# Kernel optimization log

Hardware: AMD Instinct MI355X
Metric: run time of the kernel (lower is better)

## Reference

```python
import jax, jax.numpy as jnp
import numpy as np

D = 256; H = 8; NL = 4; NP = 4; DH = D // H
IMG = 2048; SIDE = 256; NUM_INTERP = 2; PTS = NUM_INTERP + 1
SIDE_LENS = (32, 16, 8, 4)
LEVEL_SHAPES = ((256, 256), (128, 128), (64, 64), (32, 32))
IMG_STARTS = (0, 65536, 81920, 86016)   # level starts in full feature pyramid
VAL_STARTS = (0, 1024, 1280, 1344)      # level starts in cropped pyramid (sum=1360)


def layernorm(x, w, b, eps=1e-5):
    m = x.mean(-1, keepdims=True)
    v = ((x - m) ** 2).mean(-1, keepdims=True)
    return (x - m) * jax.lax.rsqrt(v + eps) * w + b


def pos_encode_2d(x, y, dim=128):
    # DETR-style sinusoidal 2D encoding: 64 dims for y, 64 for x, interleaved sin/cos
    half = dim // 2
    dim_t = 10000.0 ** (2.0 * (jnp.arange(half) // 2) / half)
    def enc(v):
        p = v[..., None] / dim_t
        return jnp.concatenate([jnp.sin(p[..., 0::2])[..., None],
                                jnp.cos(p[..., 1::2])[..., None]], -1).reshape(*v.shape, half)
    return jnp.concatenate([enc(y), enc(x)], -1)


def _forward(mask_flatten, tgt, query_pos, edge_coords, src_flatten, valid_ratios,
             in_proj_w, in_proj_b, out_proj_w, out_proj_b,
             norm1_w, norm1_b, norm2_w, norm2_b, norm3_w, norm3_b,
             lin0_w, lin0_b, lin1_w, lin1_b, lin2_w, lin2_b,
             off_w, off_b, attw_w, attw_b, val_w, val_b, oproj_w, oproj_b):
    E = tgt.shape[1]
    N = E * PTS
    # ---- self attention (dropout = identity, eval mode) ----
    qk = tgt + query_pos
    wq, wk, wv = jnp.split(in_proj_w, 3, 0)
    bq, bk, bv = jnp.split(in_proj_b, 3, 0)
    q = ((qk @ wq.T + bq) * (DH ** -0.5)).reshape(1, E, H, DH)
    k = (qk @ wk.T + bk).reshape(1, E, H, DH)
    v = (tgt @ wv.T + bv).reshape(1, E, H, DH)
    att = jax.nn.softmax(jnp.einsum('behd,bfhd->bhef', q, k), -1)
    sa = jnp.einsum('bhef,bfhd->behd', att, v).reshape(1, E, D) @ out_proj_w.T + out_proj_b
    x = layernorm(tgt + sa, norm2_w, norm2_b)

    # ---- geometry: interp points along edges, crop boxes, segment clipping ----
    a = edge_coords[0, :, :2]
    b = edge_coords[0, :, 2:]
    ts = jnp.arange(PTS, dtype=jnp.float32) / NUM_INTERP
    pts = (a[:, None, :] + ts[None, :, None] * (b - a)[:, None, :]).reshape(N, 2)
    ar = jnp.broadcast_to(a[:, None, :], (E, PTS, 2)).reshape(N, 2)
    br = jnp.broadcast_to(b[:, None, :], (E, PTS, 2)).reshape(N, 2)
    c = jnp.floor(pts).astype(jnp.int32)  # int() truncation, coords > 0
    cx, cy = c[:, 0], c[:, 1]
    minx = jnp.maximum(cx - SIDE // 2, 0)
    minx = jnp.where(minx + SIDE > IMG, IMG - SIDE, minx)
    miny = jnp.maximum(cy - SIDE // 2, 0)
    miny = jnp.where(miny + SIDE > IMG, IMG - SIDE, miny)
    fminx = minx.astype(jnp.float32)
    fminy = miny.astype(jnp.float32)
    d = br - ar
    def axis_clip(p0, d0, lo, hi):
        safe = jnp.where(d0 == 0, 1.0, d0)
        t1 = (lo - p0) / safe
        t2 = (hi - p0) / safe
        tlo = jnp.where(d0 == 0, 0.0, jnp.minimum(t1, t2))
        thi = jnp.where(d0 == 0, 1.0, jnp.maximum(t1, t2))
        return tlo, thi
    tlx, thx = axis_clip(ar[:, 0], d[:, 0], fminx, fminx + SIDE)
    tly, thy = axis_clip(ar[:, 1], d[:, 1], fminy, fminy + SIDE)
    t0 = jnp.maximum(jnp.maximum(tlx, tly), 0.0)
    t1 = jnp.maximum(jnp.minimum(jnp.minimum(thx, thy), 1.0), t0)
    ca = ar + t0[:, None] * d   # clipped segment first endpoint
    cb = ar + t1[:, None] * d   # clipped segment second endpoint
    pos_x = jnp.stack([ca[:, 0], cb[:, 0], cx.astype(jnp.float32)], -1)
    pos_y = jnp.stack([ca[:, 1], cb[:, 1], cy.astype(jnp.float32)], -1)
    pe = pos_encode_2d(pos_x, pos_y).reshape(N, -1)  # [N, 384]

    qfeat = jnp.broadcast_to((x + query_pos)[0][:, None, :], (E, PTS, D)).reshape(N, D)
    nq = jnp.concatenate([qfeat, pe], -1) @ lin0_w.T + lin0_b  # linear0, [N, 256]

    ref = jnp.stack([(cx.astype(jnp.float32) - fminx) / SIDE,
                     (cy.astype(jnp.float32) - fminy) / SIDE], -1)  # [N, 2]
    ref4 = ref[:, None, None, :] * valid_ratios[:, None]  # [N, 1, NL, 2]

    # ---- multi-level feature crops (gather) ----
    srcs, masks = [], []
    for l in range(NL):
        h, w = LEVEL_SHAPES[l]
        s = SIDE_LENS[l]
        ratio = IMG // w
        lx = jnp.round(fminx / ratio).astype(jnp.int32)
        ly = jnp.round(fminy / ratio).astype(jnp.int32)
        rows = ly[:, None] + jnp.arange(s)
        cols = lx[:, None] + jnp.arange(s)
        flat = (rows[:, :, None] * w + cols[:, None, :]).reshape(N, s * s)
        srcs.append(src_flatten[0, IMG_STARTS[l]:IMG_STARTS[l] + h * w][flat])
        masks.append(mask_flatten[0, IMG_STARTS[l]:IMG_STARTS[l] + h * w][flat])
    vsrc = jnp.concatenate(srcs, 1)    # [N, 1360, D]
    vmask = jnp.concatenate(masks, 1)  # [N, 1360]

    # ---- MSDeformAttn cross attention ----
    value = vsrc @ val_w.T + val_b
    value = jnp.where(vmask[..., None], 0.0, value).reshape(N, -1, H, DH)
    off = (nq @ off_w.T + off_b).reshape(N, H, NL, NP, 2)
    aw = jax.nn.softmax((nq @ attw_w.T + attw_b).reshape(N, H, NL * NP), -1).reshape(N, H, NL, NP)
    normalizer = jnp.array([[s, s] for s in SIDE_LENS], jnp.float32)  # (w, h) per crop level
    loc = ref4[:, 0, None, :, None, :] + off / normalizer[None, None, :, None, :]  # [N,H,NL,NP,2]
    n_idx = jnp.arange(N)[:, None, None]
    h_idx = jnp.arange(H)[None, :, None]
    out_acc = jnp.zeros((N, H, DH), jnp.float32)
    for l in range(NL):
        s = SIDE_LENS[l]
        vl = value[:, VAL_STARTS[l]:VAL_STARTS[l] + s * s].reshape(N, s, s, H, DH)
        g = loc[:, :, l]  # [N, H, NP, 2]
        px = g[..., 0] * s - 0.5  # grid_sample align_corners=False
        py = g[..., 1] * s - 0.5
        x0 = jnp.floor(px).astype(jnp.int32)
        y0 = jnp.floor(py).astype(jnp.int32)
        fx = px - x0
        fy = py - y0
        def tap(xi, yi):
            ok = (xi >= 0) & (xi < s) & (yi >= 0) & (yi < s)
            val = vl[n_idx, jnp.clip(yi, 0, s - 1), jnp.clip(xi, 0, s - 1), h_idx]
            return jnp.where(ok[..., None], val, 0.0)
        samp = (tap(x0, y0) * ((1 - fx) * (1 - fy))[..., None]
                + tap(x0 + 1, y0) * (fx * (1 - fy))[..., None]
                + tap(x0, y0 + 1) * ((1 - fx) * fy)[..., None]
                + tap(x0 + 1, y0 + 1) * (fx * fy)[..., None])  # [N,H,NP,DH]
        out_acc = out_acc + (aw[:, :, l, :, None] * samp).sum(2)
    ca_out = out_acc.reshape(N, D) @ oproj_w.T + oproj_b  # [N, D]

    # ---- per-edge mean pooling over interpolation samples ----
    pooled = ca_out.reshape(E, PTS, D).mean(1)[None]
    x = layernorm(x + pooled, norm1_w, norm1_b)
    # ---- FFN ----
    ffn = jax.nn.relu(x @ lin1_w.T + lin1_b) @ lin2_w.T + lin2_b
    return layernorm(x + ffn, norm3_w, norm3_b)


def setup_inputs():
    key = jax.random.key(0)
    ks = jax.random.split(key, 16)
    E = 128
    nrm = lambda k, shape, s=1.0: s * jax.random.normal(k, shape, jnp.float32)
    W = lambda k, o, i: nrm(k, (o, i), 0.02)
    theta = jax.random.uniform(ks[2], (E,), minval=0.0, maxval=2.0 * np.pi)
    start = jax.random.uniform(ks[3], (E, 2), minval=250.0, maxval=1798.0)
    end = start + 200.0 * jnp.stack([jnp.cos(theta), jnp.sin(theta)], -1)  # length 200 -> num_interp=2
    return dict(
        tgt=nrm(ks[0], (1, E, D)),
        query_pos=nrm(ks[1], (1, E, D)),
        edge_coords=jnp.concatenate([start, end], -1)[None],
        src_flatten=nrm(ks[4], (1, 87040, D)),
        mask_flatten=jnp.zeros((1, 87040), bool),
        valid_ratios=jnp.ones((1, 4, 2), jnp.float32),
        in_proj_w=W(ks[5], 3 * D, D), in_proj_b=jnp.zeros(3 * D),
        out_proj_w=W(ks[6], D, D), out_proj_b=jnp.zeros(D),
        norm1_w=jnp.ones(D), norm1_b=jnp.zeros(D),
        norm2_w=jnp.ones(D), norm2_b=jnp.zeros(D),
        norm3_w=jnp.ones(D), norm3_b=jnp.zeros(D),
        lin0_w=W(ks[7], D, 640), lin0_b=jnp.zeros(D),
        lin1_w=W(ks[8], 1024, D), lin1_b=jnp.zeros(1024),
        lin2_w=W(ks[9], D, 1024), lin2_b=jnp.zeros(D),
        off_w=W(ks[10], H * NL * NP * 2, D) * 0.1, off_b=jnp.zeros(H * NL * NP * 2),
        attw_w=W(ks[11], H * NL * NP, D), attw_b=jnp.zeros(H * NL * NP),
        val_w=W(ks[12], D, D), val_b=jnp.zeros(D),
        oproj_w=W(ks[13], D, D), oproj_b=jnp.zeros(D),
    )


def reference(tgt, query_pos, edge_coords, src_flatten, mask_flatten, valid_ratios,
              in_proj_w, in_proj_b, out_proj_w, out_proj_b,
              norm1_w, norm1_b, norm2_w, norm2_b, norm3_w, norm3_b,
              lin0_w, lin0_b, lin1_w, lin1_b, lin2_w, lin2_b,
              off_w, off_b, attw_w, attw_b, val_w, val_b, oproj_w, oproj_b):
    return _forward(mask_flatten, tgt, query_pos, edge_coords, src_flatten, valid_ratios,
                    in_proj_w, in_proj_b, out_proj_w, out_proj_b,
                    norm1_w, norm1_b, norm2_w, norm2_b, norm3_w, norm3_b,
                    lin0_w, lin0_b, lin1_w, lin1_b, lin2_w, lin2_b,
                    off_w, off_b, attw_w, attw_b, val_w, val_b, oproj_w, oproj_b)
```

## Files before the change

### kernel.cpp

```cpp
#include <hip/hip_runtime.h>
#include <math.h>


typedef unsigned int uint;

__device__ __forceinline__ float lo16(uint u) { return __uint_as_float(u << 16); }
__device__ __forceinline__ float hi16(uint u) { return __uint_as_float(u & 0xFFFF0000u); }
__device__ __forceinline__ uint bfr(float x) {
    uint u = __float_as_uint(x);
    return (u + 0x7FFFu + ((u >> 16) & 1u)) >> 16;
}

__device__ __forceinline__ float block_sum256f(float v, float* red) {
    int t = threadIdx.x;
    __syncthreads();
    #pragma unroll
    for (int off = 32; off; off >>= 1) v += __shfl_xor(v, off);
    if (t < 256 && (t & 63) == 0) red[t >> 6] = v;
    __syncthreads();
    return red[0] + red[1] + red[2] + red[3];
}

template <int K, int MI, int MO>
__device__ void gemm_unit(const float* __restrict__ IN, const float* __restrict__ IN2,
                          const float* __restrict__ W, const float* __restrict__ B,
                          float* __restrict__ OUT, int O, int OG, int u, float* smem) {
    constexpr int KC = 128;
    constexpr int LDT = KC + 4;
    float* tile = smem;
    int og = u % OG, rg = u / OG;
    int o0 = og * 8, r0 = rg * 64;
    int t = threadIdx.x;
    int r = t & 63;
    int ol = __builtin_amdgcn_readfirstlane(t >> 6);
    int oa = o0 + ol, ob = o0 + 4 + ol;
    const float* Wa = W + (size_t)oa * K;
    const float* Wb = W + (size_t)ob * K;
    float Ba = B[oa], Bb = B[ob];
    float acca = 0.f, accb = 0.f;
    for (int c = 0; c < K / KC; c++) {
        for (int idx = t; idx < 64 * KC; idx += 256) {
            int rr = idx >> 7, ii = idx & (KC - 1);
            int row = r0 + rr, col = c * KC + ii;
            float v;
            if (MI == 0) {
                v = IN[(size_t)row * K + col];
            } else {
                float tv = IN[row * 256 + col];
                v = (o0 < 512) ? tv + IN2[row * 256 + col] : tv;
            }
            tile[rr * LDT + ii] = v;
        }
        __syncthreads();
        const float4* wa4 = (const float4*)(Wa + c * KC);
        const float4* wb4 = (const float4*)(Wb + c * KC);
        const float4* trow = (const float4*)(tile + r * LDT);
        #pragma unroll
        for (int i4 = 0; i4 < KC / 4; i4++) {
            float4 x4 = trow[i4];
            float4 a4 = wa4[i4];
            float4 b4 = wb4[i4];
            acca += x4.x * a4.x; acca += x4.y * a4.y;
            acca += x4.z * a4.z; acca += x4.w * a4.w;
            accb += x4.x * b4.x; accb += x4.y * b4.y;
            accb += x4.z * b4.z; accb += x4.w * b4.w;
        }
        __syncthreads();
    }
    acca += Ba; accb += Bb;
    if (MO == 2) {
        if (oa < 256) acca *= 0.17677669529663687f;
        if (ob < 256) accb *= 0.17677669529663687f;
    }
    OUT[(size_t)(r0 + r) * O + oa] = acca;
    OUT[(size_t)(r0 + r) * O + ob] = accb;
}

__device__ void transpose_unit(const float* __restrict__ in, float* __restrict__ out,
                               int R, int C, int u, float* smem) {
    int TC = C >> 5;
    int tc = u % TC, tr = u / TC;
    int t = threadIdx.x;
    int lr = t >> 5, lc = t & 31;
    #pragma unroll
    for (int rr = 0; rr < 32; rr += 8)
        smem[(rr + lr) * 33 + lc] = in[(size_t)(tr * 32 + rr + lr) * C + tc * 32 + lc];
    __syncthreads();
    #pragma unroll
    for (int rr = 0; rr < 32; rr += 8)
        out[(size_t)(tc * 32 + rr + lr) * R + tr * 32 + lc] = smem[lc * 33 + rr + lr];
    __syncthreads();
}

__device__ void tpack_unit(const float* __restrict__ in, uint* __restrict__ P,
                           int C, int S, int F, int u, float* smem) {
    int TC = C >> 5;
    int tc = u % TC, tr = u / TC;
    int t = threadIdx.x;
    int lr = t >> 5, lc = t & 31;
    #pragma unroll
    for (int rr = 0; rr < 32; rr += 8)
        smem[(rr + lr) * 33 + lc] = in[(size_t)(tr * 32 + rr + lr) * C + tc * 32 + lc];
    __syncthreads();
    #pragma unroll
    for (int rep = 0; rep < 2; rep++) {
        int idx = rep * 256 + t;
        int c2 = idx >> 5, r = idx & 31;
        uint w0 = bfr(smem[r * 33 + 2 * c2]);
        uint w1 = bfr(smem[r * 33 + 2 * c2 + 1]);
        P[(size_t)(tc * 16 + c2) * S + F + tr * 32 + r] = (w1 << 16) | w0;
    }
    __syncthreads();
}

__global__ __launch_bounds__(256) void k_prep(const float* __restrict__ tgt,
                                              const float* __restrict__ qpos,
                                              const float* __restrict__ ipw,
                                              const float* __restrict__ ipb,
                                              const float* __restrict__ opw,
                                              const float* __restrict__ ojw,
                                              const float* __restrict__ valw,
                                              const float* __restrict__ l1w,
                                              const float* __restrict__ l2w,
                                              const float* __restrict__ l0w,
                                              const float* __restrict__ offw,
                                              const float* __restrict__ aww,
                                              float* __restrict__ qkv,
                                              float* __restrict__ opwT,
                                              float* __restrict__ ojwT,
                                              float* __restrict__ valwT,
                                              uint* __restrict__ Pl1,
                                              uint* __restrict__ Pl2,
                                              uint* __restrict__ Pl0,
                                              uint* __restrict__ Poaw) {
    __shared__ __align__(16) float smem[8448];
    int u = blockIdx.x;
    if (u < 192)       gemm_unit<256, 1, 2>(tgt, qpos, ipw, ipb, qkv, 768, 96, u, smem);
    else if (u < 256)  transpose_unit(opw, opwT, 256, 256, u - 192, smem);
    else if (u < 320)  transpose_unit(ojw, ojwT, 256, 256, u - 256, smem);
    else if (u < 384)  transpose_unit(valw, valwT, 256, 256, u - 320, smem);
    else if (u < 640)  tpack_unit(l1w, Pl1, 256, 1024, 0, u - 384, smem);
    else if (u < 896)  tpack_unit(l2w, Pl2, 1024, 256, 0, u - 640, smem);
    else if (u < 1056) tpack_unit(l0w, Pl0, 640, 256, 0, u - 896, smem);
    else if (u < 1120) tpack_unit(offw, Poaw, 256, 384, 0, u - 1056, smem);
    else               tpack_unit(aww, Poaw, 256, 384, 256, u - 1120, smem);
}

__device__ __forceinline__ void edge_geom(const float* __restrict__ ec, int e, int j,
                                          float* pxs, float* pys,
                                          float& fminx, float& fminy,
                                          float& cxf, float& cyf) {
    float ax = ec[e * 4 + 0], ay = ec[e * 4 + 1];
    float bx = ec[e * 4 + 2], by = ec[e * 4 + 3];
    float dx = bx - ax, dy = by - ay;
    float tj = 0.5f * (float)j;
    float ptx = __fadd_rn(ax, __fmul_rn(tj, dx));
    float pty = __fadd_rn(ay, __fmul_rn(tj, dy));
    cxf = floorf(ptx); cyf = floorf(pty);
    int minx = max((int)cxf - 128, 0); if (minx + 256 > 2048) minx = 2048 - 256;
    int miny = max((int)cyf - 128, 0); if (miny + 256 > 2048) miny = 2048 - 256;
    fminx = (float)minx; fminy = (float)miny;
    float tlx, thx, tly, thy;
    if (dx == 0.f) { tlx = 0.f; thx = 1.f; }
    else { float u1 = (fminx - ax) / dx, u2 = (fminx + 256.f - ax) / dx; tlx = fminf(u1, u2); thx = fmaxf(u1, u2); }
    if (dy == 0.f) { tly = 0.f; thy = 1.f; }
    else { float u1 = (fminy - ay) / dy, u2 = (fminy + 256.f - ay) / dy; tly = fminf(u1, u2); thy = fmaxf(u1, u2); }
    float t0 = fmaxf(fmaxf(tlx, tly), 0.f);
    float t1 = fmaxf(fminf(fminf(thx, thy), 1.f), t0);
    pxs[0] = __fadd_rn(ax, __fmul_rn(t0, dx)); pys[0] = __fadd_rn(ay, __fmul_rn(t0, dy));
    pxs[1] = __fadd_rn(ax, __fmul_rn(t1, dx)); pys[1] = __fadd_rn(ay, __fmul_rn(t1, dy));
    pxs[2] = cxf; pys[2] = cyf;
}

__global__ __launch_bounds__(1024) void k_edge(const float* __restrict__ qkv,
                                               const float* __restrict__ tgt,
                                               const float* __restrict__ qpos,
                                               const float* __restrict__ opwT,
                                               const float* __restrict__ opb,
                                               const float* __restrict__ n2w,
                                               const float* __restrict__ n2b,
                                               const float* __restrict__ ec,
                                               const uint* __restrict__ Pl0,
                                               const float* __restrict__ l0b,
                                               const uint* __restrict__ Poaw,
                                               const float* __restrict__ offb,
                                               const float* __restrict__ awb,
                                               float* __restrict__ x1,
                                               float* __restrict__ offatr,
                                               float* __restrict__ refxy,
                                               int* __restrict__ lxly) {
    int n = blockIdx.x, t = threadIdx.x;
    int e = n / 3, j = n - e * 3;
    __shared__ __align__(16) float SH[2880];
    float* xq   = SH;
    float* sq   = SH + 256;
    float* sS   = SH + 512;
    float* wred = SH + 1536;
    float* ssum = SH + 1552;
    float* srow = SH + 1560;
    float* part = SH + 1824;
    float* red  = SH + 2848;
    float* pe      = SH + 256;
    float* nrow    = SH + 640;
    float* partial = SH + 896;
    if (t < 256) sq[t] = qkv[e * 768 + t];
    __syncthreads();
    int h = t >> 7;
    {
        int f = t & 127;
        const float* kf = qkv + f * 768 + 256 + h * 32;
        const float* qh = sq + h * 32;
        float s = 0.f;
        #pragma unroll 8
        for (int d = 0; d < 32; d++) s += qh[d] * kf[d];
        float m = s;
        #pragma unroll
        for (int off = 32; off; off >>= 1) m = fmaxf(m, __shfl_xor(m, off));
        if ((t & 63) == 0) wred[t >> 6] = m;
        __syncthreads();
        float hm = fmaxf(wred[2 * h], wred[2 * h + 1]);
        float ev = __expf(s - hm);
        sS[t] = ev;
        float su = ev;
        #pragma unroll
        for (int off = 32; off; off >>= 1) su += __shfl_xor(su, off);
        if ((t & 63) == 0) wred[t >> 6] = su;
        __syncthreads();
        if (t < 8) ssum[t] = 1.f / (wred[2 * t] + wred[2 * t + 1]);
    }
    {
        int o = t & 255, c = t >> 8, hh = o >> 5, d = o & 31;
        float acc = 0.f;
        #pragma unroll 8
        for (int f = c * 32; f < c * 32 + 32; f++)
            acc += sS[hh * 128 + f] * qkv[f * 768 + 512 + hh * 32 + d];
        part[t] = acc;
    }
    __syncthreads();
    if (t < 256) srow[t] = (part[t] + part[256 + t] + part[512 + t] + part[768 + t]) * ssum[t >> 5];
    __syncthreads();
    {
        int o = t & 255, c = t >> 8;
        float acc = 0.f;
        #pragma unroll 8
        for (int i = c * 64; i < c * 64 + 64; i++) acc += srow[i] * opwT[(size_t)i * 256 + o];
        part[t] = acc;
    }
    __syncthreads();
    {
        float acc = 0.f;
        if (t < 256) acc = part[t] + part[256 + t] + part[512 + t] + part[768 + t] + opb[t] + tgt[e * 256 + t];
        float mean = block_sum256f(acc, red) * (1.f / 256.f);
        float d0 = acc - mean;
        float var = block_sum256f((t < 256) ? d0 * d0 : 0.f, red) * (1.f / 256.f);
        if (t < 256) {
            float xln = d0 * rsqrtf(var + 1e-5f) * n2w[t] + n2b[t];
            if (j == 0) x1[e * 256 + t] = xln;
            xq[t] = xln + qpos[e * 256 + t];
        }
    }
    if (t < 384) {
        float pxs[3], pys[3], fmx, fmy, cxf, cyf;
        edge_geom(ec, e, j, pxs, pys, fmx, fmy, cxf, cyf);
        int jj = t >> 7, tt = t & 127, i = tt & 63, kk = i >> 1;
        float invd = __expf(-(float)kk * (9.210340371976184f / 32.f));
        float vv = (tt < 64) ? pys[jj] : pxs[jj];
        float pp = vv * invd;
        pe[t] = (i & 1) ? __cosf(pp) : __sinf(pp);
    }
    if (t == 0) {
        float pxs[3], pys[3], fmx, fmy, cxf, cyf;
        edge_geom(ec, e, j, pxs, pys, fmx, fmy, cxf, cyf);
        refxy[n * 2 + 0] = (cxf - fmx) * (1.f / 256.f);
        refxy[n * 2 + 1] = (cyf - fmy) * (1.f / 256.f);
        lxly[n * 8 + 0] = (int)rintf(fmx * 0.125f);
        lxly[n * 8 + 1] = (int)rintf(fmx * 0.0625f);
        lxly[n * 8 + 2] = (int)rintf(fmx * 0.03125f);
        lxly[n * 8 + 3] = (int)rintf(fmx * 0.015625f);
        lxly[n * 8 + 4] = (int)rintf(fmy * 0.125f);
        lxly[n * 8 + 5] = (int)rintf(fmy * 0.0625f);
        lxly[n * 8 + 6] = (int)rintf(fmy * 0.03125f);
        lxly[n * 8 + 7] = (int)rintf(fmy * 0.015625f);
    }
    __syncthreads();
    {
        int o = t & 255, kc = t >> 8;
        float acc = 0.f;
        for (int tk = 0; tk < 10; tk++) {
            const float* inb = (tk < 4) ? (xq + tk * 64) : (pe + tk * 64 - 256);
            const uint* P = Pl0 + (size_t)tk * 8192 + (size_t)(kc * 8) * 256 + o;
            #pragma unroll
            for (int kk = 0; kk < 8; kk++) {
                uint u = P[kk * 256];
                acc += inb[(kc * 8 + kk) * 2] * lo16(u);
                acc += inb[(kc * 8 + kk) * 2 + 1] * hi16(u);
            }
        }
        partial[t] = acc;
    }
    __syncthreads();
    if (t < 256) nrow[t] = partial[t] + partial[256 + t] + partial[512 + t] + partial[768 + t] + l0b[t];
    __syncthreads();
    if (t < 768) {
        int o = t % 384, kc = t / 384;
        float acc = 0.f;
        for (int tk = 0; tk < 4; tk++) {
            const float* inb = nrow + tk * 64 + kc * 32;
            const uint* P = Poaw + (size_t)tk * 12288 + (size_t)(kc * 16) * 384 + o;
            #pragma unroll
            for (int kk = 0; kk < 16; kk++) {
                uint u = P[kk * 384];
                acc += inb[kk * 2] * lo16(u);
                acc += inb[kk * 2 + 1] * hi16(u);
            }
        }
        partial[t] = acc;
    }
    __syncthreads();
    if (t < 384) {
        float b = (t < 256) ? offb[t] : awb[t - 256];
        offatr[(size_t)n * 384 + t] = partial[t] + partial[384 + t] + b;
    }
}

__global__ __launch_bounds__(1024) void k_sample(const float* __restrict__ offatr,
                                                 const float* __restrict__ refxy,
                                                 const float* __restrict__ vr,
                                                 const int* __restrict__ lxly,
                                                 const float* __restrict__ src,
                                                 const unsigned char* __restrict__ mask,
                                                 const float* __restrict__ valwT,
                                                 const float* __restrict__ valb,
                                                 float* __restrict__ ca) {
    int n = blockIdx.x, t = threadIdx.x;
    __shared__ float sl[128];
    __shared__ float sm[8], sinv[8];
    __shared__ float sw[512];
    __shared__ int   sg[512];
    __shared__ int   rk[512];
    __shared__ int   ulist[512];
    __shared__ int   wtot[16];
    __shared__ float uw[512 * 8];
    __shared__ float agg[8 * 256];
    __shared__ float pcs[64];
    __shared__ float pagg[1024];

    if (t < 128) sl[t] = offatr[(size_t)n * 384 + 256 + t];
    #pragma unroll
    for (int z = 0; z < 4; z++) uw[z * 1024 + t] = 0.f;
    __syncthreads();
    if (t < 8) {
        float m = -1e30f;
        for (int i = 0; i < 16; i++) m = fmaxf(m, sl[t * 16 + i]);
        float s = 0.f;
        for (int i = 0; i < 16; i++) s += __expf(sl[t * 16 + i] - m);
        sm[t] = m; sinv[t] = 1.f / s;
    }
    __syncthreads();
    if (t < 512) {
        int l = t >> 7, rem = t & 127;
        int h = rem >> 4, pp = (rem >> 2) & 3, tap = t & 3;
        int s = 32 >> l, wl = 256 >> l;
        const int img_starts[4] = {0, 65536, 81920, 86016};
        float a = __expf(sl[h * 16 + l * 4 + pp] - sm[h]) * sinv[h];
        float slv = (float)s;
        float gx = refxy[n * 2 + 0] * vr[l * 2 + 0] + offatr[(size_t)n * 384 + h * 32 + l * 8 + pp * 2 + 0] / slv;
        float gy = refxy[n * 2 + 1] * vr[l * 2 + 1] + offatr[(size_t)n * 384 + h * 32 + l * 8 + pp * 2 + 1] / slv;
        float px = gx * slv - 0.5f, py = gy * slv - 0.5f;
        float x0 = floorf(px), y0 = floorf(py);
        float fx = px - x0, fy = py - y0;
        int xi = (int)x0 + (tap & 1), yi = (int)y0 + (tap >> 1);
        float wtt = ((tap & 1) ? fx : (1.f - fx)) * ((tap >> 1) ? fy : (1.f - fy));
        int g = -1;
        if (xi >= 0 && xi < s && yi >= 0 && yi < s) {
            int col = lxly[n * 8 + l] + xi;
            int row = lxly[n * 8 + 4 + l] + yi;
            g = img_starts[l] + row * wl + col;
            if (mask[g]) g = -1;
        }
        sw[t] = a * wtt;
        sg[t] = g;
    }
    __syncthreads();
    int fi = -1;
    if (t < 512) {
        int g = sg[t];
        if (g >= 0) {
            fi = t;
            int base = t & ~127;
            for (int jj = base; jj < t; jj++) if (sg[jj] == g) { fi = jj; break; }
        }
    }
    bool islead = (fi == t);
    unsigned long long bal = __ballot(islead);
    int lane = t & 63, wid = t >> 6;
    if ((t & 63) == 0) wtot[wid] = __popcll(bal);
    __syncthreads();
    int woff = 0, U = 0;
    #pragma unroll
    for (int w = 0; w < 8; w++) {
        int c = wtot[w];
        if (w < wid) woff += c;
        U += c;
    }
    if (islead) {
        int r = woff + __popcll(bal & ((1ULL << lane) - 1ULL));
        rk[t] = r;
        ulist[r] = sg[t];
    }
    __syncthreads();
    if (fi >= 0) {
        int h = (t >> 4) & 7;
        atomicAdd(&uw[rk[fi] * 8 + h], sw[t]);
    }
    __syncthreads();
    {
        int ch = t & 255, q = t >> 8;
        float a0 = 0.f, a1 = 0.f;
        for (int u = 0; u < U; u++) {
            int g = ulist[u];
            float v = src[(size_t)g * 256 + ch];
            a0 += uw[u * 8 + 2 * q] * v;
            a1 += uw[u * 8 + 2 * q + 1] * v;
        }
        agg[(2 * q) * 256 + ch] = a0;
        agg[(2 * q + 1) * 256 + ch] = a1;
    }
    if (t < 64) {
        int h = t >> 3, p = t & 7;
        float s = 0.f;
        for (int u = p; u < U; u += 8) s += uw[u * 8 + h];
        pcs[t] = s;
    }
    __syncthreads();
    {
        int h = t >> 7, rem = t & 127, o = rem & 31, kc = rem >> 5;
        const float* ag = agg + h * 256 + kc * 64;
        const float* w = valwT + (size_t)(kc * 64) * 256 + h * 32 + o;
        float pv = 0.f;
        #pragma unroll 8
        for (int i = 0; i < 64; i++) pv += ag[i] * w[(size_t)i * 256];
        pagg[t] = pv;
    }
    __syncthreads();
    if (t < 256) {
        int h = t >> 5, o = t & 31;
        float cs = pcs[h * 8 + 0] + pcs[h * 8 + 1] + pcs[h * 8 + 2] + pcs[h * 8 + 3]
                 + pcs[h * 8 + 4] + pcs[h * 8 + 5] + pcs[h * 8 + 6] + pcs[h * 8 + 7];
        float r = pagg[h * 128 + o] + pagg[h * 128 + 32 + o] + pagg[h * 128 + 64 + o] + pagg[h * 128 + 96 + o];
        ca[(size_t)n * 256 + h * 32 + o] = r + cs * valb[h * 32 + o];
    }
}

__global__ __launch_bounds__(1024) void k_tail(const float* __restrict__ ca,
                                               const float* __restrict__ x1,
                                               const float* __restrict__ ojwT,
                                               const float* __restrict__ ojb,
                                               const float* __restrict__ n1w,
                                               const float* __restrict__ n1b,
                                               const uint* __restrict__ Pl1,
                                               const float* __restrict__ l1b,
                                               const uint* __restrict__ Pl2,
                                               const float* __restrict__ l2b,
                                               const float* __restrict__ n3w,
                                               const float* __restrict__ n3b,
                                               float* __restrict__ out) {
    int e = blockIdx.x, t = threadIdx.x;
    __shared__ float row[256], red[8], x2s[256], h1s[1024], part[1024];
    if (t < 256)
        row[t] = (ca[(3 * e) * 256 + t] + ca[(3 * e + 1) * 256 + t] + ca[(3 * e + 2) * 256 + t]) * (1.f / 3.f);
    __syncthreads();
    {
        int o = t & 255, c = t >> 8;
        float acc = 0.f;
        #pragma unroll 8
        for (int i = c * 64; i < c * 64 + 64; i++) acc += row[i] * ojwT[(size_t)i * 256 + o];
        part[t] = acc;
    }
    __syncthreads();
    {
        float acc = 0.f;
        if (t < 256) acc = part[t] + part[256 + t] + part[512 + t] + part[768 + t] + ojb[t] + x1[e * 256 + t];
        float mean = block_sum256f(acc, red) * (1.f / 256.f);
        float d0 = acc - mean;
        float var = block_sum256f((t < 256) ? d0 * d0 : 0.f, red) * (1.f / 256.f);
        if (t < 256) x2s[t] = d0 * rsqrtf(var + 1e-5f) * n1w[t] + n1b[t];
    }
    __syncthreads();
    {
        float acc = l1b[t];
        #pragma unroll 8
        for (int k2 = 0; k2 < 128; k2++) {
            uint u = Pl1[(size_t)k2 * 1024 + t];
            acc += x2s[2 * k2] * lo16(u);
            acc += x2s[2 * k2 + 1] * hi16(u);
        }
        h1s[t] = fmaxf(acc, 0.f);
    }
    __syncthreads();
    {
        int o = t & 255, c = t >> 8;
        float acc = 0.f;
        #pragma unroll 8
        for (int k2 = c * 128; k2 < c * 128 + 128; k2++) {
            uint u = Pl2[(size_t)k2 * 256 + o];
            acc += h1s[2 * k2] * lo16(u);
            acc += h1s[2 * k2 + 1] * hi16(u);
        }
        part[t] = acc;
    }
    __syncthreads();
    {
        float acc = 0.f;
        if (t < 256) acc = part[t] + part[256 + t] + part[512 + t] + part[768 + t] + l2b[t] + x2s[t];
        float mean = block_sum256f(acc, red) * (1.f / 256.f);
        float d0 = acc - mean;
        float var = block_sum256f((t < 256) ? d0 * d0 : 0.f, red) * (1.f / 256.f);
        if (t < 256) out[e * 256 + t] = d0 * rsqrtf(var + 1e-5f) * n3w[t] + n3b[t];
    }
}

extern "C" void kernel_launch(void* const* d_in, const int* in_sizes, int n_in,
                              void* d_out, int out_size, void* d_ws, size_t ws_size,
                              hipStream_t stream) {
    (void)in_sizes; (void)n_in; (void)out_size; (void)ws_size;
    const float* tgt  = (const float*)d_in[0];
    const float* qpos = (const float*)d_in[1];
    const float* ec   = (const float*)d_in[2];
    const float* src  = (const float*)d_in[3];
    const unsigned char* mask = (const unsigned char*)d_in[4];
    const float* vr   = (const float*)d_in[5];
    const float* ipw  = (const float*)d_in[6];
    const float* ipb  = (const float*)d_in[7];
    const float* opw  = (const float*)d_in[8];
    const float* opb  = (const float*)d_in[9];
    const float* n1w  = (const float*)d_in[10];
    const float* n1b  = (const float*)d_in[11];
    const float* n2w  = (const float*)d_in[12];
    const float* n2b  = (const float*)d_in[13];
    const float* n3w  = (const float*)d_in[14];
    const float* n3b  = (const float*)d_in[15];
    const float* l0w  = (const float*)d_in[16];
    const float* l0b  = (const float*)d_in[17];
    const float* l1w  = (const float*)d_in[18];
    const float* l1b  = (const float*)d_in[19];
    const float* l2w  = (const float*)d_in[20];
    const float* l2b  = (const float*)d_in[21];
    const float* offw = (const float*)d_in[22];
    const float* offb = (const float*)d_in[23];
    const float* aww  = (const float*)d_in[24];
    const float* awb  = (const float*)d_in[25];
    const float* valw = (const float*)d_in[26];
    const float* valb = (const float*)d_in[27];
    const float* ojw  = (const float*)d_in[28];
    const float* ojb  = (const float*)d_in[29];

    float* ws     = (float*)d_ws;
    float* qkv    = ws;
    float* x1     = ws + 98304;
    float* offatr = ws + 131072;
    float* ca     = ws + 278528;
    float* refxy  = ws + 376832;
    int*   lxly   = (int*)(ws + 377600);
    float* opwT   = ws + 380672;
    float* ojwT   = ws + 446208;
    float* valwT  = ws + 511744;
    uint*  Pl1    = (uint*)(ws + 577280);
    uint*  Pl2    = (uint*)(ws + 708352);
    uint*  Pl0    = (uint*)(ws + 839424);
    uint*  Poaw   = (uint*)(ws + 921344);

    k_prep<<<1152, 256, 0, stream>>>(tgt, qpos, ipw, ipb, opw, ojw, valw, l1w, l2w,
                                     l0w, offw, aww,
                                     qkv, opwT, ojwT, valwT, Pl1, Pl2, Pl0, Poaw);
    k_edge<<<384, 1024, 0, stream>>>(qkv, tgt, qpos, opwT, opb, n2w, n2b, ec,
                                     Pl0, l0b, Poaw, offb, awb,
                                     x1, offatr, refxy, lxly);
    k_sample<<<384, 1024, 0, stream>>>(offatr, refxy, vr, lxly, src, mask, valwT, valb, ca);
    k_tail<<<128, 1024, 0, stream>>>(ca, x1, ojwT, ojb, n1w, n1b, Pl1, l1b, Pl2, l2b, n3w, n3b, (float*)d_out);
}
```

Measured before the change: 264.5 us.

## Fuse sampling into edge kernel and defer value projection to tail after pooling

Merges the deformable-sampling kernel into the edge kernel so offsets, attention weights, reference points and level origins stay in shared memory instead of going through global memory. The value projection is moved into the tail kernel: per-point aggregated raw features (8x256) are written out, averaged over the three points of each edge, and projected once per edge rather than once per point. This saves one launch and cuts the value-projection work by a factor of three. In exchange the intermediate buffer grows eightfold and the fused kernel needs more shared memory.

```diff
diff --git a/kernel.cpp b/kernel.cpp
--- a/kernel.cpp
+++ b/kernel.cpp
@@ -185,13 +185,15 @@
                                                const uint* __restrict__ Poaw,
                                                const float* __restrict__ offb,
                                                const float* __restrict__ awb,
+                                               const float* __restrict__ vr,
+                                               const float* __restrict__ src,
+                                               const unsigned char* __restrict__ mask,
                                                float* __restrict__ x1,
-                                               float* __restrict__ offatr,
-                                               float* __restrict__ refxy,
-                                               int* __restrict__ lxly) {
+                                               float* __restrict__ aggb,
+                                               float* __restrict__ csumb) {
     int n = blockIdx.x, t = threadIdx.x;
     int e = n / 3, j = n - e * 3;
-    __shared__ __align__(16) float SH[2880];
+    __shared__ __align__(16) float SH[5056];
     float* xq   = SH;
     float* sq   = SH + 256;
     float* sS   = SH + 512;
@@ -203,6 +205,12 @@
     float* pe      = SH + 256;
     float* nrow    = SH + 640;
     float* partial = SH + 896;
+    float* offa = SH;
+    float* sw   = SH + 384;
+    float* uw   = SH + 896;
+    float* pcs  = SH + 4992;
+    __shared__ int   sg[512], rk[512], ulist[512], wtot[16], slx[8];
+    __shared__ float sm[8], sinv[8], sref[2];
     if (t < 256) sq[t] = qkv[e * 768 + t];
     __syncthreads();
     int h = t >> 7;
@@ -271,16 +279,16 @@
     if (t == 0) {
         float pxs[3], pys[3], fmx, fmy, cxf, cyf;
         edge_geom(ec, e, j, pxs, pys, fmx, fmy, cxf, cyf);
-        refxy[n * 2 + 0] = (cxf - fmx) * (1.f / 256.f);
-        refxy[n * 2 + 1] = (cyf - fmy) * (1.f / 256.f);
-        lxly[n * 8 + 0] = (int)rintf(fmx * 0.125f);
-        lxly[n * 8 + 1] = (int)rintf(fmx * 0.0625f);
-        lxly[n * 8 + 2] = (int)rintf(fmx * 0.03125f);
-        lxly[n * 8 + 3] = (int)rintf(fmx * 0.015625f);
-        lxly[n * 8 + 4] = (int)rintf(fmy * 0.125f);
-        lxly[n * 8 + 5] = (int)rintf(fmy * 0.0625f);
-        lxly[n * 8 + 6] = (int)rintf(fmy * 0.03125f);
-        lxly[n * 8 + 7] = (int)rintf(fmy * 0.015625f);
+        sref[0] = (cxf - fmx) * (1.f / 256.f);
+        sref[1] = (cyf - fmy) * (1.f / 256.f);
+        slx[0] = (int)rintf(fmx * 0.125f);
+        slx[1] = (int)rintf(fmx * 0.0625f);
+        slx[2] = (int)rintf(fmx * 0.03125f);
+        slx[3] = (int)rintf(fmx * 0.015625f);
+        slx[4] = (int)rintf(fmy * 0.125f);
+        slx[5] = (int)rintf(fmy * 0.0625f);
+        slx[6] = (int)rintf(fmy * 0.03125f);
+        slx[7] = (int)rintf(fmy * 0.015625f);
     }
     __syncthreads();
     {
@@ -317,55 +325,33 @@
         partial[t] = acc;
     }
     __syncthreads();
+    float offav = 0.f;
     if (t < 384) {
         float b = (t < 256) ? offb[t] : awb[t - 256];
-        offatr[(size_t)n * 384 + t] = partial[t] + partial[384 + t] + b;
-    }
-}
-
-__global__ __launch_bounds__(1024) void k_sample(const float* __restrict__ offatr,
-                                                 const float* __restrict__ refxy,
-                                                 const float* __restrict__ vr,
-                                                 const int* __restrict__ lxly,
-                                                 const float* __restrict__ src,
-                                                 const unsigned char* __restrict__ mask,
-                                                 const float* __restrict__ valwT,
-                                                 const float* __restrict__ valb,
-                                                 float* __restrict__ ca) {
-    int n = blockIdx.x, t = threadIdx.x;
-    __shared__ float sl[128];
-    __shared__ float sm[8], sinv[8];
-    __shared__ float sw[512];
-    __shared__ int   sg[512];
-    __shared__ int   rk[512];
-    __shared__ int   ulist[512];
-    __shared__ int   wtot[16];
-    __shared__ float uw[512 * 8];
-    __shared__ float agg[8 * 256];
-    __shared__ float pcs[64];
-    __shared__ float pagg[1024];
-
-    if (t < 128) sl[t] = offatr[(size_t)n * 384 + 256 + t];
+        offav = partial[t] + partial[384 + t] + b;
+    }
+    __syncthreads();
+    if (t < 384) offa[t] = offav;
     #pragma unroll
     for (int z = 0; z < 4; z++) uw[z * 1024 + t] = 0.f;
     __syncthreads();
     if (t < 8) {
         float m = -1e30f;
-        for (int i = 0; i < 16; i++) m = fmaxf(m, sl[t * 16 + i]);
+        for (int i = 0; i < 16; i++) m = fmaxf(m, offa[256 + t * 16 + i]);
         float s = 0.f;
-        for (int i = 0; i < 16; i++) s += __expf(sl[t * 16 + i] - m);
+        for (int i = 0; i < 16; i++) s += __expf(offa[256 + t * 16 + i] - m);
         sm[t] = m; sinv[t] = 1.f / s;
     }
     __syncthreads();
     if (t < 512) {
         int l = t >> 7, rem = t & 127;
-        int h = rem >> 4, pp = (rem >> 2) & 3, tap = t & 3;
+        int hh = rem >> 4, pp = (rem >> 2) & 3, tap = t & 3;
         int s = 32 >> l, wl = 256 >> l;
         const int img_starts[4] = {0, 65536, 81920, 86016};
-        float a = __expf(sl[h * 16 + l * 4 + pp] - sm[h]) * sinv[h];
+        float a = __expf(offa[256 + hh * 16 + l * 4 + pp] - sm[hh]) * sinv[hh];
         float slv = (float)s;
-        float gx = refxy[n * 2 + 0] * vr[l * 2 + 0] + offatr[(size_t)n * 384 + h * 32 + l * 8 + pp * 2 + 0] / slv;
-        float gy = refxy[n * 2 + 1] * vr[l * 2 + 1] + offatr[(size_t)n * 384 + h * 32 + l * 8 + pp * 2 + 1] / slv;
+        float gx = sref[0] * vr[l * 2 + 0] + offa[hh * 32 + l * 8 + pp * 2 + 0] / slv;
+        float gy = sref[1] * vr[l * 2 + 1] + offa[hh * 32 + l * 8 + pp * 2 + 1] / slv;
         float px = gx * slv - 0.5f, py = gy * slv - 0.5f;
         float x0 = floorf(px), y0 = floorf(py);
         float fx = px - x0, fy = py - y0;
@@ -373,8 +359,8 @@
         float wtt = ((tap & 1) ? fx : (1.f - fx)) * ((tap >> 1) ? fy : (1.f - fy));
         int g = -1;
         if (xi >= 0 && xi < s && yi >= 0 && yi < s) {
-            int col = lxly[n * 8 + l] + xi;
-            int row = lxly[n * 8 + 4 + l] + yi;
+            int col = slx[l] + xi;
+            int row = slx[4 + l] + yi;
             g = img_starts[l] + row * wl + col;
             if (mask[g]) g = -1;
         }
@@ -410,8 +396,8 @@
     }
     __syncthreads();
     if (fi >= 0) {
-        int h = (t >> 4) & 7;
-        atomicAdd(&uw[rk[fi] * 8 + h], sw[t]);
+        int hh = (t >> 4) & 7;
+        atomicAdd(&uw[rk[fi] * 8 + hh], sw[t]);
     }
     __syncthreads();
     {
@@ -423,37 +409,28 @@
             a0 += uw[u * 8 + 2 * q] * v;
             a1 += uw[u * 8 + 2 * q + 1] * v;
         }
-        agg[(2 * q) * 256 + ch] = a0;
-        agg[(2 * q + 1) * 256 + ch] = a1;
+        aggb[(size_t)n * 2048 + (2 * q) * 256 + ch] = a0;
+        aggb[(size_t)n * 2048 + (2 * q + 1) * 256 + ch] = a1;
     }
     if (t < 64) {
-        int h = t >> 3, p = t & 7;
+        int hh = t >> 3, p = t & 7;
         float s = 0.f;
-        for (int u = p; u < U; u += 8) s += uw[u * 8 + h];
+        for (int u = p; u < U; u += 8) s += uw[u * 8 + hh];
         pcs[t] = s;
     }
     __syncthreads();
-    {
-        int h = t >> 7, rem = t & 127, o = rem & 31, kc = rem >> 5;
-        const float* ag = agg + h * 256 + kc * 64;
-        const float* w = valwT + (size_t)(kc * 64) * 256 + h * 32 + o;
-        float pv = 0.f;
-        #pragma unroll 8
-        for (int i = 0; i < 64; i++) pv += ag[i] * w[(size_t)i * 256];
-        pagg[t] = pv;
-    }
-    __syncthreads();
-    if (t < 256) {
-        int h = t >> 5, o = t & 31;
-        float cs = pcs[h * 8 + 0] + pcs[h * 8 + 1] + pcs[h * 8 + 2] + pcs[h * 8 + 3]
-                 + pcs[h * 8 + 4] + pcs[h * 8 + 5] + pcs[h * 8 + 6] + pcs[h * 8 + 7];
-        float r = pagg[h * 128 + o] + pagg[h * 128 + 32 + o] + pagg[h * 128 + 64 + o] + pagg[h * 128 + 96 + o];
-        ca[(size_t)n * 256 + h * 32 + o] = r + cs * valb[h * 32 + o];
-    }
-}
-
-__global__ __launch_bounds__(1024) void k_tail(const float* __restrict__ ca,
+    if (t < 8) {
+        float cs = pcs[t * 8 + 0] + pcs[t * 8 + 1] + pcs[t * 8 + 2] + pcs[t * 8 + 3]
+                 + pcs[t * 8 + 4] + pcs[t * 8 + 5] + pcs[t * 8 + 6] + pcs[t * 8 + 7];
+        csumb[n * 8 + t] = cs;
+    }
+}
+
+__global__ __launch_bounds__(1024) void k_tail(const float* __restrict__ aggb,
+                                               const float* __restrict__ csumb,
                                                const float* __restrict__ x1,
+                                               const float* __restrict__ valwT,
+                                               const float* __restrict__ valb,
                                                const float* __restrict__ ojwT,
                                                const float* __restrict__ ojb,
                                                const float* __restrict__ n1w,
@@ -466,9 +443,28 @@
                                                const float* __restrict__ n3b,
                                                float* __restrict__ out) {
     int e = blockIdx.x, t = threadIdx.x;
-    __shared__ float row[256], red[8], x2s[256], h1s[1024], part[1024];
+    __shared__ float pooledA[2048], csm[8], red[8], row[256], x2s[256], h1s[1024], part[1024];
+    #pragma unroll
+    for (int k = 0; k < 2; k++) {
+        int i = k * 1024 + t;
+        pooledA[i] = (aggb[(size_t)(3 * e) * 2048 + i] + aggb[(size_t)(3 * e + 1) * 2048 + i]
+                    + aggb[(size_t)(3 * e + 2) * 2048 + i]) * (1.f / 3.f);
+    }
+    if (t < 8)
+        csm[t] = (csumb[(3 * e) * 8 + t] + csumb[(3 * e + 1) * 8 + t] + csumb[(3 * e + 2) * 8 + t]) * (1.f / 3.f);
+    __syncthreads();
+    {
+        int o = t & 255, c = t >> 8, hh = o >> 5;
+        const float* pa = pooledA + hh * 256 + c * 64;
+        const float* w = valwT + (size_t)(c * 64) * 256 + o;
+        float acc = 0.f;
+        #pragma unroll 8
+        for (int i = 0; i < 64; i++) acc += pa[i] * w[(size_t)i * 256];
+        part[t] = acc;
+    }
+    __syncthreads();
     if (t < 256)
-        row[t] = (ca[(3 * e) * 256 + t] + ca[(3 * e + 1) * 256 + t] + ca[(3 * e + 2) * 256 + t]) * (1.f / 3.f);
+        row[t] = part[t] + part[256 + t] + part[512 + t] + part[768 + t] + csm[t >> 5] * valb[t];
     __syncthreads();
     {
         int o = t & 255, c = t >> 8;
@@ -558,24 +554,23 @@
     float* ws     = (float*)d_ws;
     float* qkv    = ws;
     float* x1     = ws + 98304;
-    float* offatr = ws + 131072;
-    float* ca     = ws + 278528;
-    float* refxy  = ws + 376832;
-    int*   lxly   = (int*)(ws + 377600);
-    float* opwT   = ws + 380672;
-    float* ojwT   = ws + 446208;
-    float* valwT  = ws + 511744;
-    uint*  Pl1    = (uint*)(ws + 577280);
-    uint*  Pl2    = (uint*)(ws + 708352);
-    uint*  Pl0    = (uint*)(ws + 839424);
-    uint*  Poaw   = (uint*)(ws + 921344);
+    float* aggb   = ws + 131072;
+    float* csumb  = ws + 917504;
+    float* opwT   = ws + 920576;
+    float* ojwT   = ws + 986112;
+    float* valwT  = ws + 1051648;
+    uint*  Pl1    = (uint*)(ws + 1117184);
+    uint*  Pl2    = (uint*)(ws + 1248256);
+    uint*  Pl0    = (uint*)(ws + 1379328);
+    uint*  Poaw   = (uint*)(ws + 1461248);
 
     k_prep<<<1152, 256, 0, stream>>>(tgt, qpos, ipw, ipb, opw, ojw, valw, l1w, l2w,
                                      l0w, offw, aww,
                                      qkv, opwT, ojwT, valwT, Pl1, Pl2, Pl0, Poaw);
     k_edge<<<384, 1024, 0, stream>>>(qkv, tgt, qpos, opwT, opb, n2w, n2b, ec,
-                                     Pl0, l0b, Poaw, offb, awb,
-                                     x1, offatr, refxy, lxly);
-    k_sample<<<384, 1024, 0, stream>>>(offatr, refxy, vr, lxly, src, mask, valwT, valb, ca);
-    k_tail<<<128, 1024, 0, stream>>>(ca, x1, ojwT, ojb, n1w, n1b, Pl1, l1b, Pl2, l2b, n3w, n3b, (float*)d_out);
-}
+                                     Pl0, l0b, Poaw, offb, awb, vr, src, mask,
+                                     x1, aggb, csumb);
+    k_tail<<<128, 1024, 0, stream>>>(aggb, csumb, x1, valwT, valb,
+                                     ojwT, ojb, n1w, n1b, Pl1, l1b, Pl2, l2b, n3w, n3b,
+                                     (float*)d_out);
+}
```

Result: no change. 265.1 us (+0.2%).
